# Kernel optimization log

Measured on AMD Instinct MI355X. Metric: run time of the kernel, lower is better.

The kernel has to match this reference:

```python
import jax, jax.numpy as jnp
import numpy as np

D_NODE, D_EDGE, D_MODEL, TOPK, N_HEADS = 64, 16, 256, 5, 4
HEAD_DIM = D_MODEL // N_HEADS


def setup_inputs() -> dict:
    key = jax.random.key(0)
    ks = jax.random.split(key, 24)
    B, N = 256, 512
    E = N - 1
    def lin(k, fi, fo):
        k1, k2 = jax.random.split(k)
        s = 1.0 / np.sqrt(fi)
        return (jax.random.uniform(k1, (fi, fo), jnp.float32, -s, s),
                jax.random.uniform(k2, (fo,), jnp.float32, -s, s))
    Wn, bn = lin(ks[0], 8, D_NODE)
    We, be = lin(ks[1], 3, D_EDGE)
    Wq, bq = lin(ks[2], D_NODE, D_MODEL)
    Wkv, bkv = lin(ks[3], 2 * D_NODE + D_EDGE, 2 * D_MODEL)
    # MultiheadAttention in/out projections (fixed shared weights)
    Wiq, biq = lin(ks[4], D_MODEL, D_MODEL)
    Wik, bik = lin(ks[5], D_MODEL, D_MODEL)
    Wiv, biv = lin(ks[6], D_MODEL, D_MODEL)
    Wo, bo = lin(ks[7], D_MODEL, D_MODEL)
    Wf1, bf1 = lin(ks[8], D_NODE + D_MODEL, D_MODEL)
    Wf2, bf2 = lin(ks[9], D_MODEL, D_MODEL)
    Ws1, bs1 = lin(ks[10], D_NODE + D_EDGE + D_MODEL, D_MODEL)
    Ws2, bs2 = lin(ks[11], D_MODEL, 1 + 6 * D_MODEL)
    node_raw = jax.random.normal(ks[12], (B, N, 8), jnp.float32)
    edge_raw = jax.random.normal(ks[13], (B, E, 3), jnp.float32)
    return dict(node_raw=node_raw, edge_raw=edge_raw, ego_id=0,
                Wn=Wn, bn=bn, We=We, be=be, Wq=Wq, bq=bq, Wkv=Wkv, bkv=bkv,
                Wiq=Wiq, biq=biq, Wik=Wik, bik=bik, Wiv=Wiv, biv=biv,
                Wo=Wo, bo=bo, Wf1=Wf1, bf1=bf1, Wf2=Wf2, bf2=bf2,
                Ws1=Ws1, bs1=bs1, Ws2=Ws2, bs2=bs2)


def reference(node_raw, edge_raw, ego_id,
              Wn, bn, We, be, Wq, bq, Wkv, bkv,
              Wiq, biq, Wik, bik, Wiv, biv, Wo, bo,
              Wf1, bf1, Wf2, bf2, Ws1, bs1, Ws2, bs2):
    B, N, _ = node_raw.shape
    E = N - 1
    ego_id = int(ego_id)
    idx = np.arange(N)
    neighbor_idx = jnp.asarray(idx[idx != ego_id])  # (E,)

    node_feat = node_raw @ Wn + bn                   # (B, N, d_node)
    edge_feat = edge_raw @ We + be                   # (B, E, d_edge)
    ego_feat = node_feat[:, ego_id]                  # (B, d_node)
    neighbor_feat = node_feat[:, neighbor_idx]       # (B, E, d_node)

    ego_bcast = jnp.broadcast_to(ego_feat[:, None, :], (B, E, D_NODE))
    edge_input = jnp.concatenate([ego_bcast, edge_feat, neighbor_feat], -1)

    Q = ego_feat @ Wq + bq                           # (B, d_model)
    kv = edge_input @ Wkv + bkv                      # (B, E, 2*d_model)
    K, V = kv[..., :D_MODEL], kv[..., D_MODEL:]

    # MultiheadAttention: single query per batch, E keys/values
    q = (Q @ Wiq + biq).reshape(B, N_HEADS, HEAD_DIM)
    k = (K @ Wik + bik).reshape(B, E, N_HEADS, HEAD_DIM)
    v = (V @ Wiv + biv).reshape(B, E, N_HEADS, HEAD_DIM)
    scores = jnp.einsum('bhd,behd->bhe', q, k) / np.sqrt(HEAD_DIM)
    attn = jax.nn.softmax(scores, axis=-1)           # (B, H, E)
    ctx = jnp.einsum('bhe,behd->bhd', attn, v).reshape(B, D_MODEL)
    c_ego = ctx @ Wo + bo                            # (B, d_model)

    h = jnp.concatenate([ego_feat, c_ego], -1)
    h_ego_prime = jax.nn.relu(h @ Wf1 + bf1) @ Wf2 + bf2  # (B, d_model)

    c_bcast = jnp.broadcast_to(c_ego[:, None, :], (B, E, D_MODEL))
    edge_input2 = jnp.concatenate([neighbor_feat, edge_feat, c_bcast], -1)
    score_out = jax.nn.relu(edge_input2 @ Ws1 + bs1) @ Ws2 + bs2  # (B,E,1+6*dm)
    score = score_out[..., 0]                        # (B, E)
    h_enc = score_out[..., 1:].reshape(B, E, 6, D_MODEL)

    topk_val, topk_idx = jax.lax.top_k(score, TOPK)  # (B, topk)
    selected = jnp.take_along_axis(h_enc, topk_idx[:, :, None, None], axis=1)
    alpha = jax.nn.softmax(topk_val, axis=-1)[:, :, None, None]  # (B,topk,1,1)
    selected = selected * alpha
    return h_ego_prime, selected, topk_idx, alpha
```

## Files before the change

### kernel.cpp

```cpp
#include <hip/hip_runtime.h>
#include <hip/hip_bf16.h>
#include <math.h>

constexpr int B = 256, NN = 512, EE = 511;

constexpr size_t F_NF    = 0;
constexpr size_t F_EF    = F_NF   + (size_t)B*NN*64;
constexpr size_t F_WCK   = F_EF   + (size_t)B*EE*16;
constexpr size_t F_BCK   = F_WCK  + 144*256;
constexpr size_t F_WCV   = F_BCK  + 256;
constexpr size_t F_BCV   = F_WCV  + 144*256;
constexpr size_t F_WQ2   = F_BCV  + 256;
constexpr size_t F_BQ2   = F_WQ2  + 64*256;
constexpr size_t F_Q     = F_BQ2  + 256;
constexpr size_t F_AW    = F_Q    + (size_t)B*256;
constexpr size_t F_C0    = F_AW   + (size_t)B*4*80;
constexpr size_t F_SC    = F_C0   + (size_t)B*4;
constexpr size_t F_US    = F_SC   + (size_t)B*4*EE;
constexpr size_t F_CEGO  = F_US   + (size_t)B*4*80;
constexpr size_t F_CVEC  = F_CEGO + (size_t)B*256;
constexpr size_t F_SC2   = F_CVEC + (size_t)B*256;
constexpr size_t F_ALPHA = F_SC2  + (size_t)B*EE;
constexpr size_t F_TKI   = F_ALPHA+ (size_t)B*5;
constexpr size_t F_HS    = F_SC;

constexpr size_t O_HEGO  = 0;
constexpr size_t O_SEL   = 65536;
constexpr size_t O_TKI   = 2031616;
constexpr size_t O_ALPHA = 2032896;

__global__ void k_fuse(const float* Wkv, const float* bkv, const float* Wik, const float* bik,
                       const float* Wiv, const float* biv, const float* Wq,  const float* bq,
                       const float* Wiq, const float* biq, float* ws){
  int t = blockIdx.x*256 + threadIdx.x;
  if (t < 36864){
    int r = t >> 8, c = t & 255;
    float a = 0.f;
    for (int m=0;m<256;m++) a += Wkv[(size_t)r*512+m] * Wik[(size_t)m*256+c];
    ws[F_WCK + t] = a;
  } else if (t < 37120){
    int c = t - 36864;
    float a = bik[c];
    for (int m=0;m<256;m++) a += bkv[m] * Wik[(size_t)m*256+c];
    ws[F_BCK + c] = a;
  } else if (t < 73984){
    int i = t - 37120; int r = i >> 8, c = i & 255;
    float a = 0.f;
    for (int m=0;m<256;m++) a += Wkv[(size_t)r*512+256+m] * Wiv[(size_t)m*256+c];
    ws[F_WCV + i] = a;
  } else if (t < 74240){
    int c = t - 73984;
    float a = biv[c];
    for (int m=0;m<256;m++) a += bkv[256+m] * Wiv[(size_t)m*256+c];
    ws[F_BCV + c] = a;
  } else if (t < 90624){
    int i = t - 74240; int r = i >> 8, c = i & 255;
    float a = 0.f;
    for (int m=0;m<256;m++) a += Wq[(size_t)r*256+m] * Wiq[(size_t)m*256+c];
    ws[F_WQ2 + i] = a;
  } else if (t < 90880){
    int c = t - 90624;
    float a = biq[c];
    for (int m=0;m<256;m++) a += bq[m] * Wiq[(size_t)m*256+c];
    ws[F_BQ2 + c] = a;
  }
}

constexpr int NFB = (B*NN*64)/256;
constexpr int EFB = (B*EE*16)/256;
__global__ void k_feat(const float* node_raw, const float* Wn, const float* bn,
                       const float* edge_raw, const float* We, const float* be, float* ws){
  int blk = blockIdx.x;
  if (blk < NFB){
    size_t t = (size_t)blk*256 + threadIdx.x;
    int j = (int)(t & 63); size_t row = t >> 6;
    float a = bn[j];
    #pragma unroll
    for (int i=0;i<8;i++) a += node_raw[row*8+i] * Wn[(size_t)i*64+j];
    ws[F_NF + t] = a;
  } else {
    size_t t = (size_t)(blk-NFB)*256 + threadIdx.x;
    int j = (int)(t & 15); size_t row = t >> 4;
    float a = be[j];
    #pragma unroll
    for (int i=0;i<3;i++) a += edge_raw[row*3+i] * We[(size_t)i*16+j];
    ws[F_EF + t] = a;
  }
}

__global__ void k_head(const int* ego_p, float* ws){
  int b = blockIdx.x >> 2, h = blockIdx.x & 3;
  int tid = threadIdx.x;
  __shared__ float qh[64];
  __shared__ float red[256];
  int ego = *ego_p;
  const float* egf = ws + F_NF + ((size_t)b*NN+ego)*64;
  if (tid < 64){
    int c = h*64 + tid;
    float a = ws[F_BQ2 + c];
    for (int i=0;i<64;i++) a += egf[i]*ws[F_WQ2 + (size_t)i*256 + c];
    qh[tid] = a;
  }
  __syncthreads();
  const float* Wck = ws + F_WCK;
  float p = 0.f;
  size_t awbase = F_AW + ((size_t)(b*4+h))*80;
  if (tid < 64){
    const float* wr = Wck + (size_t)(80+tid)*256 + h*64;
    float a=0.f; for(int d=0;d<64;d++) a += wr[d]*qh[d];
    ws[awbase + tid] = a;
  } else if (tid < 80){
    int i = tid-64;
    const float* wr = Wck + (size_t)(64+i)*256 + h*64;
    float a=0.f; for(int d=0;d<64;d++) a += wr[d]*qh[d];
    ws[awbase + 64 + i] = a;
  } else if (tid < 144){
    int j = tid-80;
    const float* wr = Wck + (size_t)j*256 + h*64;
    float a=0.f; for(int d=0;d<64;d++) a += wr[d]*qh[d];
    p = egf[j] * a;
  } else if (tid < 208){
    int d = tid-144;
    p = ws[F_BCK + h*64 + d] * qh[d];
  }
  red[tid]=p; __syncthreads();
  for (int s=128;s>0;s>>=1){ if(tid<s) red[tid]+=red[tid+s]; __syncthreads(); }
  if (tid==0) ws[F_C0 + b*4 + h] = red[0];
}

__global__ void k_scores(const int* ego_p, float* ws){
  int tile = blockIdx.x, b = blockIdx.y, tid = threadIdx.x;
  __shared__ float awz[4][80];
  __shared__ float c0s[4];
  for (int l=tid; l<320; l+=256) awz[l/80][l%80] = ws[F_AW + (size_t)b*320 + l];
  if (tid<4) c0s[tid] = ws[F_C0 + b*4 + tid];
  __syncthreads();
  int e = tile*256 + tid;
  if (e >= EE) return;
  int ego = *ego_p;
  int node = e < ego ? e : e+1;
  const float4* nr = (const float4*)(ws + F_NF + ((size_t)b*NN+node)*64);
  const float4* er = (const float4*)(ws + F_EF + ((size_t)b*EE+e)*16);
  float s[4] = {c0s[0],c0s[1],c0s[2],c0s[3]};
  #pragma unroll
  for (int i=0;i<16;i++){
    float4 x = nr[i];
    #pragma unroll
    for (int h=0;h<4;h++)
      s[h] += x.x*awz[h][i*4] + x.y*awz[h][i*4+1] + x.z*awz[h][i*4+2] + x.w*awz[h][i*4+3];
  }
  #pragma unroll
  for (int i=0;i<4;i++){
    float4 x = er[i];
    #pragma unroll
    for (int h=0;h<4;h++)
      s[h] += x.x*awz[h][64+i*4] + x.y*awz[h][64+i*4+1] + x.z*awz[h][64+i*4+2] + x.w*awz[h][64+i*4+3];
  }
  #pragma unroll
  for (int h=0;h<4;h++) ws[F_SC + ((size_t)(b*4+h))*EE + e] = s[h]*0.125f;
}

__global__ __launch_bounds__(256) void k_attn(const int* ego_p, float* ws){
  int b = blockIdx.x, tid = threadIdx.x;
  int h = tid >> 6, lane = tid & 63;
  __shared__ float sc[4][512];
  __shared__ float tnf[32][64];
  __shared__ float tef[32][16];
  const float* s = ws + F_SC + ((size_t)(b*4+h))*EE;
  float v[8];
  float mx = -INFINITY;
  #pragma unroll
  for (int j=0;j<8;j++){
    int e = lane + j*64;
    v[j] = (e<EE) ? s[e] : -INFINITY;
    mx = fmaxf(mx, v[j]);
  }
  #pragma unroll
  for (int m=32;m>0;m>>=1) mx = fmaxf(mx, __shfl_xor(mx, m, 64));
  float sum = 0.f;
  #pragma unroll
  for (int j=0;j<8;j++){
    int e = lane + j*64;
    float ev = (e<EE) ? expf(v[j]-mx) : 0.f;
    v[j] = ev; sum += ev;
  }
  #pragma unroll
  for (int m=32;m>0;m>>=1) sum += __shfl_xor(sum, m, 64);
  float inv = 1.f/sum;
  #pragma unroll
  for (int j=0;j<8;j++) sc[h][lane + j*64] = v[j]*inv;
  __syncthreads();
  int ego = *ego_p;
  float accn = 0.f;
  float acce = 0.f;
  for (int t0=0; t0<EE; t0+=32){
    __syncthreads();
    for (int q=tid; q<512; q+=256){
      int e = t0 + (q>>4), c4 = q & 15;
      float4 val = make_float4(0.f,0.f,0.f,0.f);
      if (e < EE){
        int node = e<ego ? e : e+1;
        val = *(const float4*)(ws + F_NF + ((size_t)b*NN+node)*64 + c4*4);
      }
      *(float4*)&tnf[q>>4][c4*4] = val;
    }
    if (tid < 128){
      int e = t0 + (tid>>2), c4 = tid & 3;
      float4 val = make_float4(0.f,0.f,0.f,0.f);
      if (e < EE) val = *(const float4*)(ws + F_EF + ((size_t)b*EE+e)*16 + c4*4);
      *(float4*)&tef[tid>>2][c4*4] = val;
    }
    __syncthreads();
    #pragma unroll 8
    for (int e=0;e<32;e++){
      float a = sc[h][t0+e];
      accn = fmaf(a, tnf[e][lane], accn);
      if (lane < 16) acce = fmaf(a, tef[e][lane], acce);
    }
  }
  ws[F_US + ((size_t)(b*4+h))*80 + lane] = accn;
  if (lane < 16) ws[F_US + ((size_t)(b*4+h))*80 + 64 + lane] = acce;
}

__global__ void k_bfinal(const int* ego_p,
                         const float* Wo, const float* bo,
                         const float* Wf1, const float* bf1p,
                         const float* Wf2, const float* bf2p,
                         const float* Ws1, const float* bs1,
                         float* ws, float* out){
  int b = blockIdx.x, t = threadIdx.x;
  __shared__ float ego_s[64], us_s[4][80], ctx_s[256], cego_s[256], hf_s[256];
  int ego = *ego_p;
  if (t < 64) ego_s[t] = ws[F_NF + ((size_t)b*NN+ego)*64 + t];
  for (int l=t; l<320; l+=256) us_s[l/80][l%80] = ws[F_US + (size_t)b*320 + l];
  __syncthreads();
  {
    int h = t >> 6;
    const float* Wcv = ws + F_WCV;
    float a = ws[F_BCV + t];
    for (int i=0;i<64;i++) a += ego_s[i]*Wcv[(size_t)i*256+t];
    for (int i=0;i<16;i++) a += us_s[h][64+i]*Wcv[(size_t)(64+i)*256+t];
    for (int i=0;i<64;i++) a += us_s[h][i]*Wcv[(size_t)(80+i)*256+t];
    ctx_s[t]=a;
  }
  __syncthreads();
  {
    float a = bo[t];
    for (int i=0;i<256;i++) a += ctx_s[i]*Wo[(size_t)i*256+t];
    cego_s[t]=a; ws[F_CEGO + (size_t)b*256+t]=a;
  }
  __syncthreads();
  {
    float a = bf1p[t];
    for (int i=0;i<64;i++)  a += ego_s[i]*Wf1[(size_t)i*256+t];
    for (int i=0;i<256;i++) a += cego_s[i]*Wf1[(size_t)(64+i)*256+t];
    hf_s[t]=fmaxf(a,0.f);
  }
  __syncthreads();
  {
    float a = bf2p[t];
    for (int i=0;i<256;i++) a += hf_s[i]*Wf2[(size_t)i*256+t];
    out[O_HEGO + (size_t)b*256+t] = a;
  }
  {
    float a = bs1[t];
    for (int i=0;i<256;i++) a += cego_s[i]*Ws1[(size_t)(80+i)*256+t];
    ws[F_CVEC + (size_t)b*256+t]=a;
  }
}

__global__ __launch_bounds__(512) void k_bigscore(const int* ego_p, const float* Ws1,
                                                  const float* Ws2, const float* bs2, float* ws){
  int tile = blockIdx.x, b = blockIdx.y;
  int tid = threadIdx.x;
  __shared__ float Fe[64][80];
  __shared__ float Bs[16][256];
  __shared__ float cv_s[256], w2_s[256];
  int ego = *ego_p;
  if (tid < 256){
    cv_s[tid] = ws[F_CVEC + (size_t)b*256 + tid];
    w2_s[tid] = Ws2[(size_t)tid*1537];
  }
  for (int l=tid; l<80*64; l+=512){
    int e = l/80, k = l - e*80;
    int eg = tile*64 + e;
    float v = 0.f;
    if (eg < EE){
      int node = eg<ego?eg:eg+1;
      v = (k<64) ? ws[F_NF + ((size_t)b*NN+node)*64 + k]
                 : ws[F_EF + ((size_t)b*EE+eg)*16 + (k-64)];
    }
    Fe[e][k] = v;
  }
  int tc = tid & 31, te = tid >> 5;
  float acc[4][8];
  #pragma unroll
  for (int i=0;i<4;i++)
    #pragma unroll
    for (int j=0;j<8;j++) acc[i][j]=0.f;

  for (int c=0;c<5;c++){
    __syncthreads();
    {
      float4* dst = (float4*)&Bs[0][0];
      const float4* s4 = (const float4*)(Ws1 + (size_t)(c*16)*256);
      dst[tid]       = s4[tid];
      dst[tid + 512] = s4[tid + 512];
    }
    __syncthreads();
    #pragma unroll
    for (int kk=0; kk<16; kk+=4){
      float A[4][4];
      #pragma unroll
      for (int i=0;i<4;i++){
        float4 t4 = *(const float4*)&Fe[te*4+i][c*16+kk];
        A[i][0]=t4.x; A[i][1]=t4.y; A[i][2]=t4.z; A[i][3]=t4.w;
      }
      #pragma unroll
      for (int q=0;q<4;q++){
        float4 b0 = *(const float4*)&Bs[kk+q][tc*4];
        float4 b1 = *(const float4*)&Bs[kk+q][128 + tc*4];
        float bw[8] = {b0.x,b0.y,b0.z,b0.w,b1.x,b1.y,b1.z,b1.w};
        #pragma unroll
        for (int i=0;i<4;i++)
          #pragma unroll
          for (int j=0;j<8;j++) acc[i][j] = fmaf(A[i][q], bw[j], acc[i][j]);
      }
    }
  }
  float bs20 = bs2[0];
  #pragma unroll
  for (int i=0;i<4;i++){
    float p = 0.f;
    #pragma unroll
    for (int j=0;j<4;j++){
      int col = tc*4 + j;
      float hcol = acc[i][j] + cv_s[col];
      p += fmaxf(hcol,0.f)*w2_s[col];
    }
    #pragma unroll
    for (int j=0;j<4;j++){
      int col = 128 + tc*4 + j;
      float hcol = acc[i][4+j] + cv_s[col];
      p += fmaxf(hcol,0.f)*w2_s[col];
    }
    #pragma unroll
    for (int m=16;m>0;m>>=1) p += __shfl_xor(p, m, 64);
    if (tc==0){
      int eg = tile*64 + te*4 + i;
      if (eg < EE) ws[F_SC2 + (size_t)b*EE + eg] = p + bs20;
    }
  }
}

__global__ void k_topk(float* ws, float* out){
  int b = blockIdx.x, tid = threadIdx.x;
  __shared__ float sv[256]; __shared__ int si[256];
  __shared__ float tv[8];   __shared__ int tix[8];
  const float* s = ws + F_SC2 + (size_t)b*EE;
  float v0 = tid<EE ? s[tid] : -INFINITY;       int i0 = tid;
  float v1 = (tid+256)<EE ? s[tid+256] : -INFINITY; int i1 = tid+256;
  for (int t=0;t<5;t++){
    float bvv; int bii;
    if (v0 > v1 || (v0==v1 && i0<i1)){ bvv=v0; bii=i0; } else { bvv=v1; bii=i1; }
    sv[tid]=bvv; si[tid]=bii; __syncthreads();
    for (int st=128; st>0; st>>=1){
      if (tid<st){
        float ov=sv[tid+st]; int oi=si[tid+st];
        if (ov > sv[tid] || (ov==sv[tid] && oi<si[tid])){ sv[tid]=ov; si[tid]=oi; }
      }
      __syncthreads();
    }
    if (tid==0){ tv[t]=sv[0]; tix[t]=si[0]; }
    __syncthreads();
    int w = tix[t];
    if (i0==w) v0=-INFINITY;
    if (i1==w) v1=-INFINITY;
    __syncthreads();
  }
  if (tid==0){
    float m = tv[0];
    float ex[5]; float sum=0.f;
    for (int t=0;t<5;t++){ ex[t]=expf(tv[t]-m); sum+=ex[t]; }
    for (int t=0;t<5;t++){
      float al = ex[t]/sum;
      ws[F_ALPHA + (size_t)b*5+t] = al;
      ((int*)(ws + F_TKI))[b*5+t] = tix[t];
      out[O_TKI   + (size_t)b*5+t] = (float)tix[t];
      out[O_ALPHA + (size_t)b*5+t] = al;
    }
  }
}

__global__ void k_hid(const int* ego_p, const float* Ws1, float* ws){
  int bt = blockIdx.x;
  int b = bt/5;
  int tid = threadIdx.x;
  __shared__ float fr[80];
  int e = ((const int*)(ws+F_TKI))[bt];
  int ego = *ego_p;
  int node = e<ego ? e : e+1;
  if (tid < 64)      fr[tid] = ws[F_NF + ((size_t)b*NN+node)*64 + tid];
  else if (tid < 80) fr[tid] = ws[F_EF + ((size_t)b*EE+e)*16 + (tid-64)];
  __syncthreads();
  float a = ws[F_CVEC + (size_t)b*256 + tid];
  for (int d=0;d<80;d++) a += fr[d]*Ws1[(size_t)d*256+tid];
  ws[F_HS + (size_t)bt*256 + tid] = fmaxf(a,0.f);
}

__global__ __launch_bounds__(256) void k_enc(const float* Ws2, const float* bs2,
                                             float* ws, float* out){
  int r = blockIdx.x, g = blockIdx.y, tid = threadIdx.x;
  int n = r*256 + tid;
  __shared__ float hs[10][256];
  __shared__ float al[10];
  int b0 = g*2;
  for (int l=tid; l<10*256; l+=256)
    hs[l>>8][l&255] = ws[F_HS + ((size_t)b0*5)*256 + l];
  if (tid<10) al[tid] = ws[F_ALPHA + (size_t)b0*5 + tid];
  __syncthreads();
  float acc[10];
  #pragma unroll
  for (int i=0;i<10;i++) acc[i]=0.f;
  const float* w2p = Ws2 + 1 + n;
  for (int j=0;j<256;j+=4){
    float w0 = w2p[(size_t)(j+0)*1537];
    float w1 = w2p[(size_t)(j+1)*1537];
    float w2 = w2p[(size_t)(j+2)*1537];
    float w3 = w2p[(size_t)(j+3)*1537];
    #pragma unroll
    for (int i=0;i<10;i++){
      float4 h = *(const float4*)&hs[i][j];
      acc[i] = fmaf(h.x,w0, fmaf(h.y,w1, fmaf(h.z,w2, fmaf(h.w,w3, acc[i]))));
    }
  }
  float bb = bs2[1+n];
  #pragma unroll
  for (int i=0;i<10;i++)
    out[O_SEL + ((size_t)(b0*5+i))*1536 + n] = (acc[i]+bb)*al[i];
}

extern "C" void kernel_launch(void* const* d_in, const int* in_sizes, int n_in,
                              void* d_out, int out_size, void* d_ws, size_t ws_size,
                              hipStream_t stream){
  const float* node_raw=(const float*)d_in[0];
  const float* edge_raw=(const float*)d_in[1];
  const int*  ego_p   =(const int*)d_in[2];
  const float* Wn =(const float*)d_in[3];  const float* bn =(const float*)d_in[4];
  const float* We =(const float*)d_in[5];  const float* be =(const float*)d_in[6];
  const float* Wq =(const float*)d_in[7];  const float* bq =(const float*)d_in[8];
  const float* Wkv=(const float*)d_in[9];  const float* bkv=(const float*)d_in[10];
  const float* Wiq=(const float*)d_in[11]; const float* biq=(const float*)d_in[12];
  const float* Wik=(const float*)d_in[13]; const float* bik=(const float*)d_in[14];
  const float* Wiv=(const float*)d_in[15]; const float* biv=(const float*)d_in[16];
  const float* Wo =(const float*)d_in[17]; const float* bo =(const float*)d_in[18];
  const float* Wf1=(const float*)d_in[19]; const float* bf1p=(const float*)d_in[20];
  const float* Wf2=(const float*)d_in[21]; const float* bf2p=(const float*)d_in[22];
  const float* Ws1=(const float*)d_in[23]; const float* bs1=(const float*)d_in[24];
  const float* Ws2=(const float*)d_in[25]; const float* bs2=(const float*)d_in[26];
  float* ws=(float*)d_ws;
  float* out=(float*)d_out;

  k_fuse<<<355,256,0,stream>>>(Wkv,bkv,Wik,bik,Wiv,biv,Wq,bq,Wiq,biq,ws);
  k_feat<<<NFB+EFB,256,0,stream>>>(node_raw,Wn,bn,edge_raw,We,be,ws);
  k_head<<<B*4,256,0,stream>>>(ego_p,ws);
  k_scores<<<dim3(2,B),256,0,stream>>>(ego_p,ws);
  k_attn<<<B,256,0,stream>>>(ego_p,ws);
  k_bfinal<<<B,256,0,stream>>>(ego_p,Wo,bo,Wf1,bf1p,Wf2,bf2p,Ws1,bs1,ws,out);
  k_bigscore<<<dim3(8,B),512,0,stream>>>(ego_p,Ws1,Ws2,bs2,ws);
  k_topk<<<B,256,0,stream>>>(ws,out);
  k_hid<<<B*5,256,0,stream>>>(ego_p,Ws1,ws);
  k_enc<<<dim3(6,128),256,0,stream>>>(Ws2,bs2,ws,out);
}
```

Before: 251.6 us.

## Split-K parallelize weight fusion and per-batch MLP; warp-level top-k

The weight-fusion kernel now splits each 256-long dot product across four groups of 64 threads and reduces through shared memory, giving four times as many blocks. The per-batch final MLP kernel goes from 256 to 1024 threads, with each matvec split along K into four partial sums reduced in shared memory. Top-k now runs one 64-lane warp per batch, using registers and shuffles instead of block-wide shared-memory reductions with many barriers. The aim is better GPU occupancy on these small, latency-bound kernels, at the cost of extra reductions and synchronisation.

```diff
diff --git a/kernel.cpp b/kernel.cpp
--- a/kernel.cpp
+++ b/kernel.cpp
@@ -29,40 +29,44 @@
 constexpr size_t O_TKI   = 2031616;
 constexpr size_t O_ALPHA = 2032896;
 
-__global__ void k_fuse(const float* Wkv, const float* bkv, const float* Wik, const float* bik,
+__global__ __launch_bounds__(256) void k_fuse(const float* Wkv, const float* bkv,
+                       const float* Wik, const float* bik,
                        const float* Wiv, const float* biv, const float* Wq,  const float* bq,
                        const float* Wiq, const float* biq, float* ws){
-  int t = blockIdx.x*256 + threadIdx.x;
-  if (t < 36864){
-    int r = t >> 8, c = t & 255;
-    float a = 0.f;
-    for (int m=0;m<256;m++) a += Wkv[(size_t)r*512+m] * Wik[(size_t)m*256+c];
-    ws[F_WCK + t] = a;
-  } else if (t < 37120){
-    int c = t - 36864;
-    float a = bik[c];
-    for (int m=0;m<256;m++) a += bkv[m] * Wik[(size_t)m*256+c];
-    ws[F_BCK + c] = a;
-  } else if (t < 73984){
-    int i = t - 37120; int r = i >> 8, c = i & 255;
-    float a = 0.f;
-    for (int m=0;m<256;m++) a += Wkv[(size_t)r*512+256+m] * Wiv[(size_t)m*256+c];
-    ws[F_WCV + i] = a;
-  } else if (t < 74240){
-    int c = t - 73984;
-    float a = biv[c];
-    for (int m=0;m<256;m++) a += bkv[256+m] * Wiv[(size_t)m*256+c];
-    ws[F_BCV + c] = a;
-  } else if (t < 90624){
-    int i = t - 74240; int r = i >> 8, c = i & 255;
-    float a = 0.f;
-    for (int m=0;m<256;m++) a += Wq[(size_t)r*256+m] * Wiq[(size_t)m*256+c];
-    ws[F_WQ2 + i] = a;
-  } else if (t < 90880){
-    int c = t - 90624;
-    float a = biq[c];
-    for (int m=0;m<256;m++) a += bq[m] * Wiq[(size_t)m*256+c];
-    ws[F_BQ2 + c] = a;
+  int o = threadIdx.x & 63, ks = threadIdx.x >> 6;
+  int g = blockIdx.x*64 + o;
+  int m0 = ks*64;
+  float a = 0.f;
+  if (g < 36864){
+    int r = g >> 8, c = g & 255;
+    for (int m=m0; m<m0+64; m++) a += Wkv[(size_t)r*512+m] * Wik[(size_t)m*256+c];
+  } else if (g < 37120){
+    int c = g - 36864;
+    for (int m=m0; m<m0+64; m++) a += bkv[m] * Wik[(size_t)m*256+c];
+  } else if (g < 73984){
+    int i = g - 37120; int r = i >> 8, c = i & 255;
+    for (int m=m0; m<m0+64; m++) a += Wkv[(size_t)r*512+256+m] * Wiv[(size_t)m*256+c];
+  } else if (g < 74240){
+    int c = g - 73984;
+    for (int m=m0; m<m0+64; m++) a += bkv[256+m] * Wiv[(size_t)m*256+c];
+  } else if (g < 90624){
+    int i = g - 74240; int r = i >> 8, c = i & 255;
+    for (int m=m0; m<m0+64; m++) a += Wq[(size_t)r*256+m] * Wiq[(size_t)m*256+c];
+  } else if (g < 90880){
+    int c = g - 90624;
+    for (int m=m0; m<m0+64; m++) a += bq[m] * Wiq[(size_t)m*256+c];
+  }
+  __shared__ float red[256];
+  red[threadIdx.x] = a;
+  __syncthreads();
+  if (ks == 0 && g < 90880){
+    float s = red[o] + red[64+o] + red[128+o] + red[192+o];
+    if (g < 36864)      ws[F_WCK + g] = s;
+    else if (g < 37120) ws[F_BCK + (g-36864)] = s + bik[g-36864];
+    else if (g < 73984) ws[F_WCV + (g-37120)] = s;
+    else if (g < 74240) ws[F_BCV + (g-73984)] = s + biv[g-73984];
+    else if (g < 90624) ws[F_WQ2 + (g-74240)] = s;
+    else                ws[F_BQ2 + (g-90624)] = s + biq[g-90624];
   }
 }
 
@@ -222,50 +226,64 @@
   if (lane < 16) ws[F_US + ((size_t)(b*4+h))*80 + 64 + lane] = acce;
 }
 
-__global__ void k_bfinal(const int* ego_p,
+__global__ __launch_bounds__(1024) void k_bfinal(const int* ego_p,
                          const float* Wo, const float* bo,
                          const float* Wf1, const float* bf1p,
                          const float* Wf2, const float* bf2p,
                          const float* Ws1, const float* bs1,
                          float* ws, float* out){
-  int b = blockIdx.x, t = threadIdx.x;
+  int b = blockIdx.x;
+  int tid = threadIdx.x;
+  int t = tid & 255, ks = tid >> 8;
   __shared__ float ego_s[64], us_s[4][80], ctx_s[256], cego_s[256], hf_s[256];
+  __shared__ float red[1024], red2[1024];
   int ego = *ego_p;
-  if (t < 64) ego_s[t] = ws[F_NF + ((size_t)b*NN+ego)*64 + t];
-  for (int l=t; l<320; l+=256) us_s[l/80][l%80] = ws[F_US + (size_t)b*320 + l];
+  if (tid < 64) ego_s[tid] = ws[F_NF + ((size_t)b*NN+ego)*64 + tid];
+  if (tid >= 64 && tid < 384){ int l = tid-64; us_s[l/80][l%80] = ws[F_US + (size_t)b*320 + l]; }
   __syncthreads();
   {
     int h = t >> 6;
-    const float* Wcv = ws + F_WCV;
-    float a = ws[F_BCV + t];
-    for (int i=0;i<64;i++) a += ego_s[i]*Wcv[(size_t)i*256+t];
-    for (int i=0;i<16;i++) a += us_s[h][64+i]*Wcv[(size_t)(64+i)*256+t];
-    for (int i=0;i<64;i++) a += us_s[h][i]*Wcv[(size_t)(80+i)*256+t];
-    ctx_s[t]=a;
-  }
+    float a = 0.f;
+    for (int j=ks*36; j<ks*36+36; j++){
+      float x = (j<64) ? ego_s[j] : (j<80 ? us_s[h][j] : us_s[h][j-80]);
+      a += x * ws[F_WCV + (size_t)j*256 + t];
+    }
+    red[tid] = a;
+  }
+  __syncthreads();
+  if (ks==0) ctx_s[t] = ws[F_BCV+t] + red[t]+red[256+t]+red[512+t]+red[768+t];
   __syncthreads();
   {
-    float a = bo[t];
-    for (int i=0;i<256;i++) a += ctx_s[i]*Wo[(size_t)i*256+t];
-    cego_s[t]=a; ws[F_CEGO + (size_t)b*256+t]=a;
-  }
+    float a = 0.f;
+    for (int i=ks*64; i<ks*64+64; i++) a += ctx_s[i]*Wo[(size_t)i*256+t];
+    red[tid] = a;
+  }
+  __syncthreads();
+  if (ks==0) cego_s[t] = bo[t] + red[t]+red[256+t]+red[512+t]+red[768+t];
   __syncthreads();
   {
-    float a = bf1p[t];
-    for (int i=0;i<64;i++)  a += ego_s[i]*Wf1[(size_t)i*256+t];
-    for (int i=0;i<256;i++) a += cego_s[i]*Wf1[(size_t)(64+i)*256+t];
-    hf_s[t]=fmaxf(a,0.f);
-  }
+    float a = 0.f;
+    for (int j=ks*80; j<ks*80+80; j++){
+      float x = (j<64) ? ego_s[j] : cego_s[j-64];
+      a += x * Wf1[(size_t)j*256+t];
+    }
+    red[tid] = a;
+  }
+  __syncthreads();
+  if (ks==0) hf_s[t] = fmaxf(bf1p[t] + red[t]+red[256+t]+red[512+t]+red[768+t], 0.f);
   __syncthreads();
   {
-    float a = bf2p[t];
-    for (int i=0;i<256;i++) a += hf_s[i]*Wf2[(size_t)i*256+t];
-    out[O_HEGO + (size_t)b*256+t] = a;
-  }
-  {
-    float a = bs1[t];
-    for (int i=0;i<256;i++) a += cego_s[i]*Ws1[(size_t)(80+i)*256+t];
-    ws[F_CVEC + (size_t)b*256+t]=a;
+    float a=0.f, c=0.f;
+    for (int i=ks*64; i<ks*64+64; i++){
+      a += hf_s[i]*Wf2[(size_t)i*256+t];
+      c += cego_s[i]*Ws1[(size_t)(80+i)*256+t];
+    }
+    red[tid]=a; red2[tid]=c;
+  }
+  __syncthreads();
+  if (ks==0){
+    out[O_HEGO + (size_t)b*256+t] = bf2p[t] + red[t]+red[256+t]+red[512+t]+red[768+t];
+    ws[F_CVEC + (size_t)b*256+t]  = bs1[t]  + red2[t]+red2[256+t]+red2[512+t]+red2[768+t];
   }
 }
 
@@ -353,41 +371,49 @@
   }
 }
 
-__global__ void k_topk(float* ws, float* out){
-  int b = blockIdx.x, tid = threadIdx.x;
-  __shared__ float sv[256]; __shared__ int si[256];
-  __shared__ float tv[8];   __shared__ int tix[8];
+__global__ __launch_bounds__(256) void k_topk(float* ws, float* out){
+  int w = threadIdx.x >> 6, lane = threadIdx.x & 63;
+  int b = blockIdx.x*4 + w;
   const float* s = ws + F_SC2 + (size_t)b*EE;
-  float v0 = tid<EE ? s[tid] : -INFINITY;       int i0 = tid;
-  float v1 = (tid+256)<EE ? s[tid+256] : -INFINITY; int i1 = tid+256;
-  for (int t=0;t<5;t++){
-    float bvv; int bii;
-    if (v0 > v1 || (v0==v1 && i0<i1)){ bvv=v0; bii=i0; } else { bvv=v1; bii=i1; }
-    sv[tid]=bvv; si[tid]=bii; __syncthreads();
-    for (int st=128; st>0; st>>=1){
-      if (tid<st){
-        float ov=sv[tid+st]; int oi=si[tid+st];
-        if (ov > sv[tid] || (ov==sv[tid] && oi<si[tid])){ sv[tid]=ov; si[tid]=oi; }
-      }
-      __syncthreads();
-    }
-    if (tid==0){ tv[t]=sv[0]; tix[t]=si[0]; }
-    __syncthreads();
-    int w = tix[t];
-    if (i0==w) v0=-INFINITY;
-    if (i1==w) v1=-INFINITY;
-    __syncthreads();
-  }
-  if (tid==0){
-    float m = tv[0];
-    float ex[5]; float sum=0.f;
-    for (int t=0;t<5;t++){ ex[t]=expf(tv[t]-m); sum+=ex[t]; }
-    for (int t=0;t<5;t++){
-      float al = ex[t]/sum;
-      ws[F_ALPHA + (size_t)b*5+t] = al;
-      ((int*)(ws + F_TKI))[b*5+t] = tix[t];
-      out[O_TKI   + (size_t)b*5+t] = (float)tix[t];
-      out[O_ALPHA + (size_t)b*5+t] = al;
+  float v[8];
+  #pragma unroll
+  for (int j=0;j<8;j++){
+    int e = lane + j*64;
+    v[j] = (e<EE) ? s[e] : -INFINITY;
+  }
+  float tv[5]; int tix[5];
+  #pragma unroll 5
+  for (int tsel=0; tsel<5; tsel++){
+    float bv = -INFINITY; int bi = 1<<30;
+    #pragma unroll
+    for (int j=0;j<8;j++){
+      int e = lane + j*64;
+      if (v[j] > bv || (v[j]==bv && e < bi)){ bv=v[j]; bi=e; }
+    }
+    #pragma unroll
+    for (int m=32;m>0;m>>=1){
+      float ov = __shfl_xor(bv, m, 64);
+      int   oi = __shfl_xor(bi, m, 64);
+      if (ov > bv || (ov==bv && oi < bi)){ bv=ov; bi=oi; }
+    }
+    tv[tsel]=bv; tix[tsel]=bi;
+    if ((bi & 63) == lane){
+      int jj = bi >> 6;
+      #pragma unroll
+      for (int j=0;j<8;j++) if (j==jj) v[j] = -INFINITY;
+    }
+  }
+  if (lane==0){
+    float m = tv[0], ex[5], sum=0.f;
+    #pragma unroll
+    for (int t2=0;t2<5;t2++){ ex[t2]=expf(tv[t2]-m); sum+=ex[t2]; }
+    #pragma unroll
+    for (int t2=0;t2<5;t2++){
+      float al = ex[t2]/sum;
+      ws[F_ALPHA + (size_t)b*5+t2] = al;
+      ((int*)(ws + F_TKI))[b*5+t2] = tix[t2];
+      out[O_TKI   + (size_t)b*5+t2] = (float)tix[t2];
+      out[O_ALPHA + (size_t)b*5+t2] = al;
     }
   }
 }
@@ -461,14 +487,14 @@
   float* ws=(float*)d_ws;
   float* out=(float*)d_out;
 
-  k_fuse<<<355,256,0,stream>>>(Wkv,bkv,Wik,bik,Wiv,biv,Wq,bq,Wiq,biq,ws);
+  k_fuse<<<1420,256,0,stream>>>(Wkv,bkv,Wik,bik,Wiv,biv,Wq,bq,Wiq,biq,ws);
   k_feat<<<NFB+EFB,256,0,stream>>>(node_raw,Wn,bn,edge_raw,We,be,ws);
   k_head<<<B*4,256,0,stream>>>(ego_p,ws);
   k_scores<<<dim3(2,B),256,0,stream>>>(ego_p,ws);
   k_attn<<<B,256,0,stream>>>(ego_p,ws);
-  k_bfinal<<<B,256,0,stream>>>(ego_p,Wo,bo,Wf1,bf1p,Wf2,bf2p,Ws1,bs1,ws,out);
+  k_bfinal<<<B,1024,0,stream>>>(ego_p,Wo,bo,Wf1,bf1p,Wf2,bf2p,Ws1,bs1,ws,out);
   k_bigscore<<<dim3(8,B),512,0,stream>>>(ego_p,Ws1,Ws2,bs2,ws);
-  k_topk<<<B,256,0,stream>>>(ws,out);
+  k_topk<<<64,256,0,stream>>>(ws,out);
   k_hid<<<B*5,256,0,stream>>>(ego_p,Ws1,ws);
   k_enc<<<dim3(6,128),256,0,stream>>>(Ws2,bs2,ws,out);
 }
```

Measured after the change: 271.2 us. +7.8%, slower.
